# Performance work log

Measured on AMD Instinct MI355X. Metric: run time of the kernel, lower is better.

## Reference

```python
import jax, jax.numpy as jnp
import numpy as np

N_NODES = 50000
N_EDGES = 600000
IN_DIM = 128


def _glorot(key, shape, fan_in, fan_out):
    lim = float(np.sqrt(6.0 / (fan_in + fan_out)))
    return jax.random.uniform(key, shape, jnp.float32, -lim, lim)


def setup_inputs() -> dict:
    key = jax.random.key(0)
    ks = jax.random.split(key, 16)
    x = jax.random.normal(ks[0], (N_NODES, IN_DIM), jnp.float32)
    src = jax.random.randint(ks[1], (N_EDGES,), 0, N_NODES)
    off = jax.random.randint(ks[2], (N_EDGES,), 1, N_NODES)
    dst = (src + off) % N_NODES  # guarantees src != dst
    edge_index = jnp.stack([src, dst]).astype(jnp.int64)
    weights = jax.random.normal(ks[3], (N_EDGES,), jnp.float32)
    # layer 1: GATv2Conv(128, 64, heads=2) -> out 128 (concat)
    Wl1 = _glorot(ks[4], (128, 128), 128, 128)
    bl1 = jnp.zeros((128,), jnp.float32)
    Wr1 = _glorot(ks[5], (128, 128), 128, 128)
    br1 = jnp.zeros((128,), jnp.float32)
    att1 = _glorot(ks[6], (2, 64), 64, 64)
    bias1 = jnp.zeros((128,), jnp.float32)
    # layer 2: GATv2Conv(128, 4, heads=1, concat=False)
    Wl2 = _glorot(ks[7], (128, 4), 128, 4)
    bl2 = jnp.zeros((4,), jnp.float32)
    Wr2 = _glorot(ks[8], (128, 4), 128, 4)
    br2 = jnp.zeros((4,), jnp.float32)
    att2 = _glorot(ks[9], (1, 4), 4, 4)
    bias2 = jnp.zeros((4,), jnp.float32)
    return dict(x=x, edge_index=edge_index, weights=weights,
                Wl1=Wl1, bl1=bl1, Wr1=Wr1, br1=br1, att1=att1, bias1=bias1,
                Wl2=Wl2, bl2=bl2, Wr2=Wr2, br2=br2, att2=att2, bias2=bias2)


def gatv2_layer(x, src, dst, Wl, bl, Wr, br, att, bias, heads, ch, concat):
    # PyG GATv2Conv, eval mode (attention dropout off).
    N = x.shape[0]
    xl = (x @ Wl + bl).reshape(N, heads, ch)  # source transform (messages)
    xr = (x @ Wr + br).reshape(N, heads, ch)  # target transform
    e = xl[src] + xr[dst]                     # [E, H, C]
    e = jnp.where(e > 0, e, 0.2 * e)          # leaky_relu, negative_slope=0.2
    alpha = jnp.einsum('ehc,hc->eh', e, att)  # [E, H]
    amax = jax.ops.segment_max(alpha, dst, num_segments=N)
    amax = jnp.where(jnp.isfinite(amax), amax, 0.0)
    ex = jnp.exp(alpha - amax[dst])
    denom = jax.ops.segment_sum(ex, dst, num_segments=N)
    a = ex / (denom[dst] + 1e-16)             # segment softmax over in-edges
    out = jax.ops.segment_sum(a[:, :, None] * xl[src], dst, num_segments=N)
    out = out.reshape(N, heads * ch) if concat else out.mean(axis=1)
    return out + bias


def reference(x, edge_index, weights,
              Wl1, bl1, Wr1, br1, att1, bias1,
              Wl2, bl2, Wr2, br2, att2, bias2):
    N = x.shape[0]
    loop = jnp.arange(N, dtype=edge_index.dtype)
    src = jnp.concatenate([edge_index[0], loop])  # add self loops
    dst = jnp.concatenate([edge_index[1], loop])
    h = gatv2_layer(x, src, dst, Wl1, bl1, Wr1, br1, att1, bias1,
                    heads=2, ch=64, concat=True)
    h = jnp.where(h > 0, h, 0.01 * h)  # nn.LeakyReLU default slope 0.01
    h = gatv2_layer(h, src, dst, Wl2, bl2, Wr2, br2, att2, bias2,
                    heads=1, ch=4, concat=False)
    return jax.nn.softmax(h, axis=1)
```

## Files before the change

### kernel.cpp

```cpp
#include <hip/hip_runtime.h>

#define N_NODES 50000
#define N_EDGES 600000
#define E_TOT   650000
#define EBLK    2540
#define MAXD    64

typedef __attribute__((ext_vector_type(8))) short short8;
typedef __attribute__((ext_vector_type(4))) float f32x4;

__device__ inline short f2bf(float f) {
  union { float f; unsigned u; } v; v.f = f;
  unsigned r = (v.u + 0x7FFFu + ((v.u >> 16) & 1u)) >> 16;
  return (short)r;
}
__device__ inline float bf2f(short u) {
  union { unsigned u; float f; } v; v.u = ((unsigned)(unsigned short)u) << 16;
  return v.f;
}


__global__ __launch_bounds__(256) void build_kernel(
    const int* __restrict__ ei, int* __restrict__ deg, int* __restrict__ ell,
    const float* __restrict__ Wl, const float* __restrict__ Wr, short* __restrict__ Wbf) {
  int b = blockIdx.x;
  if (b < EBLK) {
    int e = b * 256 + threadIdx.x;
    if (e >= E_TOT) return;
    int s, d;
    if (e < N_EDGES) { s = ei[e]; d = ei[N_EDGES + e]; }
    else             { s = e - N_EDGES; d = s; }
    int pos = atomicAdd(&deg[d], 1);
    ell[d * MAXD + pos] = s;
  } else {
    int gid = (b - EBLK) * 256 + threadIdx.x;
    int c = gid >> 4, k8 = (gid & 15) * 8;
    const float* W = (c < 128) ? Wl : Wr;
    int cc = c & 127;
    short8 o;
    #pragma unroll
    for (int j = 0; j < 8; ++j) o[j] = f2bf(W[(size_t)(k8 + j) * 128 + cc]);
    *(short8*)(Wbf + (size_t)c * 128 + k8) = o;
  }
}


#define LSWZ(row, k) (((row) * 128 + (k)) ^ (((row) & 7) << 3))

__global__ __launch_bounds__(256) void gemm1_mfma(
    const float* __restrict__ x, const short* __restrict__ Wbf,
    const float* __restrict__ bl, const float* __restrict__ br,
    short* __restrict__ xl, short* __restrict__ xr) {
  __shared__ short As[128 * 128];
  __shared__ short Bs[128 * 128];
  int t = threadIdx.x;
  int row0 = blockIdx.x * 128;

  #pragma unroll
  for (int i = 0; i < 8; ++i) {
    int c = t + 256 * i;
    int r = c >> 4, k8 = (c & 15) * 8;
    int gr = row0 + r;
    short8 o = {};
    if (gr < N_NODES) {
      const float* p = x + (size_t)gr * 128 + k8;
      f32x4 a = *(const f32x4*)p, b = *(const f32x4*)(p + 4);
      o[0] = f2bf(a.x); o[1] = f2bf(a.y); o[2] = f2bf(a.z); o[3] = f2bf(a.w);
      o[4] = f2bf(b.x); o[5] = f2bf(b.y); o[6] = f2bf(b.z); o[7] = f2bf(b.w);
    }
    *(short8*)(&As[LSWZ(r, k8)]) = o;
  }

  int w = t >> 6, lane = t & 63;
  int wm = (w >> 1) * 64, wn = (w & 1) * 64;
  int lr = lane & 15, lk = (lane >> 4) * 8;

  for (int hb = 0; hb < 2; ++hb) {
    #pragma unroll
    for (int i = 0; i < 8; ++i) {
      int c = t + 256 * i;
      int col = c >> 4, k8 = (c & 15) * 8;
      short8 o = *(const short8*)(Wbf + (size_t)(hb * 128 + col) * 128 + k8);
      *(short8*)(&Bs[LSWZ(col, k8)]) = o;
    }
    __syncthreads();

    f32x4 acc[4][4];
    #pragma unroll
    for (int m = 0; m < 4; ++m)
      #pragma unroll
      for (int n = 0; n < 4; ++n) acc[m][n] = (f32x4){0.f, 0.f, 0.f, 0.f};

    #pragma unroll
    for (int ks = 0; ks < 4; ++ks) {
      int k0 = ks * 32 + lk;
      short8 af[4], bfr[4];
      #pragma unroll
      for (int m = 0; m < 4; ++m) {
        int r = wm + m * 16 + lr;
        af[m] = *(const short8*)(&As[LSWZ(r, k0)]);
      }
      #pragma unroll
      for (int n = 0; n < 4; ++n) {
        int r = wn + n * 16 + lr;
        bfr[n] = *(const short8*)(&Bs[LSWZ(r, k0)]);
      }
      #pragma unroll
      for (int m = 0; m < 4; ++m)
        #pragma unroll
        for (int n = 0; n < 4; ++n)
          acc[m][n] = __builtin_amdgcn_mfma_f32_16x16x32_bf16(af[m], bfr[n], acc[m][n], 0, 0, 0);
    }

    const float* B0 = hb ? br : bl;
    short* O = hb ? xr : xl;
    int orow = (lane >> 4) * 4;
    #pragma unroll
    for (int n = 0; n < 4; ++n) {
      int col = wn + n * 16 + lr;
      float bv = B0[col];
      #pragma unroll
      for (int m = 0; m < 4; ++m) {
        #pragma unroll
        for (int r = 0; r < 4; ++r) {
          int grow = row0 + wm + m * 16 + orow + r;
          if (grow < N_NODES) O[(size_t)grow * 128 + col] = f2bf(acc[m][n][r] + bv);
        }
      }
    }
    __syncthreads();
  }
}


__global__ __launch_bounds__(256) void agg1_fused(
    const short* __restrict__ xl1, const short* __restrict__ xr1,
    const float* __restrict__ att, const float* __restrict__ bias,
    const float* __restrict__ Wl2, const float* __restrict__ bl2,
    const float* __restrict__ Wr2, const float* __restrict__ br2,
    const int* __restrict__ deg, const int* __restrict__ ell,
    float* __restrict__ xl2, float* __restrict__ xr2) {
  __shared__ short sbuf[4][8][512];
  int gid = blockIdx.x * 256 + threadIdx.x;
  int node = gid >> 4;
  int t = threadIdx.x;
  int wid = t >> 6, lane = t & 63;
  int L = lane & 15;
  int gbase = lane & 48;

  short8 xr8 = *(const short8*)(xr1 + (size_t)node * 128 + L * 8);
  float xr[8], at[8];
  #pragma unroll
  for (int r = 0; r < 8; ++r) xr[r] = bf2f(xr8[r]);
  *(float4*)(at)     = *(const float4*)(att + L * 8);
  *(float4*)(at + 4) = *(const float4*)(att + L * 8 + 4);

  float m = -1e30f, denom = 0.f;
  float acc[8];
  #pragma unroll
  for (int r = 0; r < 8; ++r) acc[r] = 0.f;

  int p1 = deg[node];
  const int* erow = ell + (size_t)node * MAXD;

  for (int base = 0; base < p1; base += 8) {
    int pE = base + L;
    int myidx = erow[pE < p1 ? pE : p1 - 1];
    #pragma unroll
    for (int j = 0; j < 8; ++j) {
      int ij = __shfl(myidx, gbase + j);
      const short* gp = xl1 + (size_t)ij * 128 + L * 8;
      __builtin_amdgcn_global_load_lds(
          (const __attribute__((address_space(1))) void*)gp,
          (__attribute__((address_space(3))) void*)&sbuf[wid][j][0],
          16, 0, 0);
    }
    asm volatile("s_waitcnt vmcnt(0)" ::: "memory");
    __builtin_amdgcn_sched_barrier(0);

    float pa[8];
    #pragma unroll
    for (int j = 0; j < 8; ++j) {
      short8 v = *(const short8*)(&sbuf[wid][j][lane * 8]);
      float s = 0.f;
      #pragma unroll
      for (int r = 0; r < 8; ++r) {
        float e = bf2f(v[r]) + xr[r];
        e = fmaxf(e, 0.2f * e);
        s = fmaf(e, at[r], s);
      }
      pa[j] = s;
    }
    #pragma unroll
    for (int st = 1; st < 8; st <<= 1) {
      #pragma unroll
      for (int j = 0; j < 8; ++j) pa[j] += __shfl_xor(pa[j], st);
    }
    #pragma unroll
    for (int j = 0; j < 8; ++j) pa[j] = (base + j < p1) ? pa[j] : -1e30f;
    float bm = pa[0];
    #pragma unroll
    for (int j = 1; j < 8; ++j) bm = fmaxf(bm, pa[j]);
    float mnew  = fmaxf(m, bm);
    float scale = __expf(m - mnew);
    float wgt[8], dsum = 0.f;
    #pragma unroll
    for (int j = 0; j < 8; ++j) { wgt[j] = __expf(pa[j] - mnew); dsum += wgt[j]; }
    denom = denom * scale + dsum;
    #pragma unroll
    for (int r = 0; r < 8; ++r) acc[r] *= scale;
    #pragma unroll
    for (int j = 0; j < 8; ++j) {
      short8 v = *(const short8*)(&sbuf[wid][j][lane * 8]);
      #pragma unroll
      for (int r = 0; r < 8; ++r) acc[r] = fmaf(wgt[j], bf2f(v[r]), acc[r]);
    }
    m = mnew;
  }

  float inv = 1.f / (denom + 1e-16f);
  float o[8];
  #pragma unroll
  for (int r = 0; r < 8; ++r) {
    float v = acc[r] * inv + bias[L * 8 + r];
    o[r] = fmaxf(v, 0.01f * v);
  }
  float pl[4] = {0.f, 0.f, 0.f, 0.f}, pr[4] = {0.f, 0.f, 0.f, 0.f};
  #pragma unroll
  for (int r = 0; r < 8; ++r) {
    float4 wl = *(const float4*)(Wl2 + (size_t)(L * 8 + r) * 4);
    float4 wr = *(const float4*)(Wr2 + (size_t)(L * 8 + r) * 4);
    pl[0] += o[r] * wl.x;  pl[1] += o[r] * wl.y;  pl[2] += o[r] * wl.z;  pl[3] += o[r] * wl.w;
    pr[0] += o[r] * wr.x;  pr[1] += o[r] * wr.y;  pr[2] += o[r] * wr.z;  pr[3] += o[r] * wr.w;
  }
  #pragma unroll
  for (int off = 1; off < 16; off <<= 1) {
    #pragma unroll
    for (int c = 0; c < 4; ++c) {
      pl[c] += __shfl_xor(pl[c], off);
      pr[c] += __shfl_xor(pr[c], off);
    }
  }
  if (L == 0) {
    float4 b0 = *(const float4*)(bl2);
    float4 b1 = *(const float4*)(br2);
    *(float4*)(xl2 + (size_t)node * 4) =
        make_float4(pl[0] + b0.x, pl[1] + b0.y, pl[2] + b0.z, pl[3] + b0.w);
    *(float4*)(xr2 + (size_t)node * 4) =
        make_float4(pr[0] + b1.x, pr[1] + b1.y, pr[2] + b1.z, pr[3] + b1.w);
  }
}


__global__ __launch_bounds__(256) void agg2_kernel(
    const float* __restrict__ xl2, const float* __restrict__ xr2,
    const float* __restrict__ att, const float* __restrict__ bias,
    const int* __restrict__ deg, const int* __restrict__ ell,
    float* __restrict__ out) {
  int gid = blockIdx.x * 256 + threadIdx.x;
  int node = gid >> 4;
  if (node >= N_NODES) return;
  int L = threadIdx.x & 15;
  float4 xr = *(const float4*)(xr2 + (size_t)node * 4);
  float4 at = *(const float4*)(att);
  float m = -1e30f, denom = 0.f;
  float4 acc = make_float4(0.f, 0.f, 0.f, 0.f);
  int p1 = deg[node];
  const int* erow = ell + (size_t)node * MAXD;
  int nit = (p1 + 15) >> 4;
  int p = L;
  for (int it = 0; it < nit; ++it) {
    bool valid = p < p1;
    int s = erow[valid ? p : p1 - 1];
    float4 xv = *(const float4*)(xl2 + (size_t)s * 4);
    float e0 = xv.x + xr.x; e0 = fmaxf(e0, 0.2f * e0);
    float e1 = xv.y + xr.y; e1 = fmaxf(e1, 0.2f * e1);
    float e2 = xv.z + xr.z; e2 = fmaxf(e2, 0.2f * e2);
    float e3 = xv.w + xr.w; e3 = fmaxf(e3, 0.2f * e3);
    float pa = e0 * at.x + e1 * at.y + e2 * at.z + e3 * at.w;
    pa = valid ? pa : -1e30f;
    float mnew  = fmaxf(m, pa);
    float scale = __expf(m - mnew);
    float wgt   = __expf(pa - mnew);
    denom = denom * scale + wgt;
    acc.x = acc.x * scale + wgt * xv.x;
    acc.y = acc.y * scale + wgt * xv.y;
    acc.z = acc.z * scale + wgt * xv.z;
    acc.w = acc.w * scale + wgt * xv.w;
    m = mnew;
    p += 16;
  }
  #pragma unroll
  for (int off = 1; off < 16; off <<= 1) {
    float mo = __shfl_xor(m, off);
    float dn = __shfl_xor(denom, off);
    float ax = __shfl_xor(acc.x, off);
    float ay = __shfl_xor(acc.y, off);
    float az = __shfl_xor(acc.z, off);
    float aw = __shfl_xor(acc.w, off);
    float mnew = fmaxf(m, mo);
    float sa = __expf(m - mnew);
    float sb = __expf(mo - mnew);
    denom = denom * sa + dn * sb;
    acc.x = acc.x * sa + ax * sb;
    acc.y = acc.y * sa + ay * sb;
    acc.z = acc.z * sa + az * sb;
    acc.w = acc.w * sa + aw * sb;
    m = mnew;
  }
  if (L == 0) {
    float inv = 1.f / (denom + 1e-16f);
    float4 b = *(const float4*)(bias);
    float o0 = acc.x * inv + b.x;
    float o1 = acc.y * inv + b.y;
    float o2 = acc.z * inv + b.z;
    float o3 = acc.w * inv + b.w;
    float mx = fmaxf(fmaxf(o0, o1), fmaxf(o2, o3));
    float q0 = __expf(o0 - mx), q1 = __expf(o1 - mx), q2 = __expf(o2 - mx), q3 = __expf(o3 - mx);
    float r = 1.f / (q0 + q1 + q2 + q3);
    *(float4*)(out + (size_t)node * 4) = make_float4(q0 * r, q1 * r, q2 * r, q3 * r);
  }
}


extern "C" void kernel_launch(void* const* d_in, const int* in_sizes, int n_in,
                              void* d_out, int out_size, void* d_ws, size_t ws_size,
                              hipStream_t stream) {
  (void)in_sizes; (void)n_in; (void)out_size; (void)ws_size;
  const float* x     = (const float*)d_in[0];
  const int*   ei    = (const int*)d_in[1];
  const float* Wl1   = (const float*)d_in[3];
  const float* bl1   = (const float*)d_in[4];
  const float* Wr1   = (const float*)d_in[5];
  const float* br1   = (const float*)d_in[6];
  const float* att1  = (const float*)d_in[7];
  const float* bias1 = (const float*)d_in[8];
  const float* Wl2   = (const float*)d_in[9];
  const float* bl2   = (const float*)d_in[10];
  const float* Wr2   = (const float*)d_in[11];
  const float* br2   = (const float*)d_in[12];
  const float* att2  = (const float*)d_in[13];
  const float* bias2 = (const float*)d_in[14];
  float* out = (float*)d_out;

  char* w = (char*)d_ws;
  auto alloc = [&](size_t bytes) -> char* {
    char* p = w;
    w += (bytes + 255) & ~(size_t)255;
    return p;
  };
  short* xl1    = (short*)alloc((size_t)N_NODES * 128 * 2);
  short* xr1    = (short*)alloc((size_t)N_NODES * 128 * 2);
  float* xl2    = (float*)alloc((size_t)N_NODES * 4 * 4);
  float* xr2    = (float*)alloc((size_t)N_NODES * 4 * 4);
  int*   deg    = (int*)alloc((size_t)N_NODES * 4);
  int*   ell    = (int*)alloc((size_t)N_NODES * MAXD * 4);
  short* Wbf    = (short*)alloc((size_t)256 * 128 * 2);

  hipMemsetAsync(deg, 0, (size_t)N_NODES * 4, stream);

  build_kernel<<<EBLK + 16, 256, 0, stream>>>(ei, deg, ell, Wl1, Wr1, Wbf);
  gemm1_mfma<<<(N_NODES + 127) / 128, 256, 0, stream>>>(x, Wbf, bl1, br1, xl1, xr1);
  agg1_fused<<<(N_NODES * 16 + 255) / 256, 256, 0, stream>>>(
      xl1, xr1, att1, bias1, Wl2, bl2, Wr2, br2, deg, ell, xl2, xr2);
  agg2_kernel<<<(N_NODES * 16 + 255) / 256, 256, 0, stream>>>(
      xl2, xr2, att2, bias2, deg, ell, out);
}
```

Measured before the change: 141.3 us.

## Fold memset into init kernel and co-schedule edge build with GEMM

Replaces the hipMemsetAsync of the degree array with zeroing blocks inside a small init kernel that also converts the weights to bf16. The edge-list ELL build (atomic degree counting and scatter) moves out of its own kernel and becomes extra blocks of the GEMM launch, so the latency-bound scatter can overlap with the MFMA GEMM. This removes one launch and one memset. The GEMM blocks still declare large shared memory, so the build blocks carry the same LDS footprint and may limit occupancy for the scatter work.

```diff
diff --git a/kernel.cpp b/kernel.cpp
--- a/kernel.cpp
+++ b/kernel.cpp
@@ -4,6 +4,8 @@
 #define N_EDGES 600000
 #define E_TOT   650000
 #define EBLK    2540
+#define GBLK    391
+#define ZBLK    196
 #define MAXD    64
 
 typedef __attribute__((ext_vector_type(8))) short short8;
@@ -20,20 +22,15 @@
 }
 
 
-__global__ __launch_bounds__(256) void build_kernel(
-    const int* __restrict__ ei, int* __restrict__ deg, int* __restrict__ ell,
+__global__ __launch_bounds__(256) void init_kernel(
+    int* __restrict__ deg,
     const float* __restrict__ Wl, const float* __restrict__ Wr, short* __restrict__ Wbf) {
   int b = blockIdx.x;
-  if (b < EBLK) {
-    int e = b * 256 + threadIdx.x;
-    if (e >= E_TOT) return;
-    int s, d;
-    if (e < N_EDGES) { s = ei[e]; d = ei[N_EDGES + e]; }
-    else             { s = e - N_EDGES; d = s; }
-    int pos = atomicAdd(&deg[d], 1);
-    ell[d * MAXD + pos] = s;
+  if (b < ZBLK) {
+    int i = b * 256 + threadIdx.x;
+    if (i < N_NODES) deg[i] = 0;
   } else {
-    int gid = (b - EBLK) * 256 + threadIdx.x;
+    int gid = (b - ZBLK) * 256 + threadIdx.x;
     int c = gid >> 4, k8 = (gid & 15) * 8;
     const float* W = (c < 128) ? Wl : Wr;
     int cc = c & 127;
@@ -47,13 +44,27 @@
 
 #define LSWZ(row, k) (((row) * 128 + (k)) ^ (((row) & 7) << 3))
 
-__global__ __launch_bounds__(256) void gemm1_mfma(
+__global__ __launch_bounds__(256) void gemm_build(
     const float* __restrict__ x, const short* __restrict__ Wbf,
     const float* __restrict__ bl, const float* __restrict__ br,
-    short* __restrict__ xl, short* __restrict__ xr) {
+    short* __restrict__ xl, short* __restrict__ xr,
+    const int* __restrict__ ei, int* __restrict__ deg, int* __restrict__ ell) {
   __shared__ short As[128 * 128];
   __shared__ short Bs[128 * 128];
   int t = threadIdx.x;
+
+  if (blockIdx.x >= GBLK) {
+    int e = (blockIdx.x - GBLK) * 256 + t;
+    if (e < E_TOT) {
+      int s, d;
+      if (e < N_EDGES) { s = ei[e]; d = ei[N_EDGES + e]; }
+      else             { s = e - N_EDGES; d = s; }
+      int pos = atomicAdd(&deg[d], 1);
+      ell[d * MAXD + pos] = s;
+    }
+    return;
+  }
+
   int row0 = blockIdx.x * 128;
 
   #pragma unroll
@@ -357,10 +368,8 @@
   int*   ell    = (int*)alloc((size_t)N_NODES * MAXD * 4);
   short* Wbf    = (short*)alloc((size_t)256 * 128 * 2);
 
-  hipMemsetAsync(deg, 0, (size_t)N_NODES * 4, stream);
-
-  build_kernel<<<EBLK + 16, 256, 0, stream>>>(ei, deg, ell, Wl1, Wr1, Wbf);
-  gemm1_mfma<<<(N_NODES + 127) / 128, 256, 0, stream>>>(x, Wbf, bl1, br1, xl1, xr1);
+  init_kernel<<<ZBLK + 16, 256, 0, stream>>>(deg, Wl1, Wr1, Wbf);
+  gemm_build<<<GBLK + EBLK, 256, 0, stream>>>(x, Wbf, bl1, br1, xl1, xr1, ei, deg, ell);
   agg1_fused<<<(N_NODES * 16 + 255) / 256, 256, 0, stream>>>(
       xl1, xr1, att1, bias1, Wl2, bl2, Wr2, br2, deg, ell, xl2, xr2);
   agg2_kernel<<<(N_NODES * 16 + 255) / 256, 256, 0, stream>>>(
```

Result: faster. 128.2 us (-9.3%).
